# Kernel tuning notes

Hardware: AMD Instinct MI355X
Metric: run time of the kernel (lower is better)

## Reference

```python
import jax, jax.numpy as jnp
import numpy as np

N_NODES = 65536   # N
D_HID   = 128     # D (hidden)
N_GROUPS = 16384  # G portfolios
GROUP_LEN = 64    # lines per portfolio (port_len entries)
N_LINES = N_GROUPS * GROUP_LEN  # L
BATCH = 16384     # B samples


def setup_inputs() -> dict:
    key = jax.random.key(0)
    k = jax.random.split(key, 5)
    H = jax.random.normal(k[0], (N_NODES, D_HID), dtype=jnp.float32)
    port_w_signed_flat = jax.random.normal(k[1], (N_LINES,), dtype=jnp.float32)
    anchor_idx = jax.random.randint(k[2], (BATCH,), 0, N_NODES, dtype=jnp.int32)
    pf_gid = jax.random.randint(k[3], (BATCH,), 0, N_GROUPS, dtype=jnp.int32)
    port_nodes_flat = jax.random.randint(k[4], (N_LINES,), 0, N_NODES, dtype=jnp.int32)
    port_len = jnp.full((N_GROUPS,), GROUP_LEN, dtype=jnp.int32)
    return {
        'H': H,
        'port_w_signed_flat': port_w_signed_flat,
        'anchor_idx': anchor_idx,
        'pf_gid': pf_gid,
        'port_nodes_flat': port_nodes_flat,
        'port_len': port_len,
    }


def reference(H, port_w_signed_flat, anchor_idx, pf_gid, port_nodes_flat, port_len):
    """Faithful, vectorized port of compute_samplewise_portfolio_vectors_loo.

    Ragged segment-weighted mean per portfolio group, with strict leave-one-out
    correction for each sample's anchor node, followed by L2 normalization.
    Returns (V_abs, V_sgn), each [B, D].
    """
    N, D = H.shape
    G = port_len.shape[0]
    L = port_nodes_flat.shape[0]

    # gid per flat line: repeat_interleave(arange(G), lens)
    gid_lines = jnp.repeat(jnp.arange(G, dtype=jnp.int32), port_len,
                           total_repeat_length=L)

    w_abs = jnp.abs(port_w_signed_flat)
    Hl = H[port_nodes_flat]                                  # [L, D] gather
    S_abs = jax.ops.segment_sum(w_abs[:, None] * Hl, gid_lines, num_segments=G)
    W_abs = jax.ops.segment_sum(w_abs, gid_lines, num_segments=G)
    W_sgn = jax.ops.segment_sum(port_w_signed_flat, gid_lines, num_segments=G)

    valid = (pf_gid >= 0) & (pf_gid < G)
    g = jnp.clip(pf_gid, 0, G - 1)

    # Leave-one-out self-weight: sum of w over lines where (gid==g_i, node==anchor_i).
    # Vectorized join via a sorted composite int32 key (G*N < 2^31 by construction).
    keys_l = gid_lines * N + port_nodes_flat                 # [L]
    keys_s = g * N + anchor_idx                              # [B]
    order = jnp.argsort(keys_l)
    sk = keys_l[order]
    zero1 = jnp.zeros((1,), H.dtype)
    ca = jnp.concatenate([zero1, jnp.cumsum(w_abs[order])])
    cs = jnp.concatenate([zero1, jnp.cumsum(port_w_signed_flat[order])])
    lo = jnp.searchsorted(sk, keys_s, side='left')
    hi = jnp.searchsorted(sk, keys_s, side='right')
    self_w_abs = ca[hi] - ca[lo]                             # [B]
    self_w_sgn = cs[hi] - cs[lo]                             # [B]

    Ha = H[anchor_idx]                                       # [B, D]
    denom = jnp.maximum(W_abs[g] - self_w_abs, 1e-12)        # clamp_min
    V_abs = (S_abs[g] - self_w_abs[:, None] * Ha) / denom[:, None]
    V_sgn = ((W_sgn[g] - self_w_sgn) / denom)[:, None] * V_abs

    V_abs = jnp.where(valid[:, None], V_abs, jnp.zeros((), H.dtype))
    V_sgn = jnp.where(valid[:, None], V_sgn, jnp.zeros((), H.dtype))

    # torch F.normalize: x / clamp(||x||, min=eps)
    na = jnp.linalg.norm(V_abs, axis=1, keepdims=True)
    V_abs = V_abs / jnp.maximum(na, 1e-6)
    ns = jnp.linalg.norm(V_sgn, axis=1, keepdims=True)
    V_sgn = jnp.where(ns > 0, V_sgn / jnp.maximum(ns, 1e-6), V_sgn)
    return V_abs, V_sgn
```

## Files before the change

### kernel.cpp

```cpp
#include <hip/hip_runtime.h>
#include <hip/hip_bf16.h>


#define DDIM 128

__device__ inline unsigned bf_rne(float x) {
    unsigned u = __float_as_uint(x);
    return (u + 0x7FFFu + ((u >> 16) & 1u)) >> 16;
}

__device__ inline void unpack2(unsigned d, float& lo, float& hi) {
    lo = __uint_as_float(d << 16);
    hi = __uint_as_float(d & 0xFFFF0000u);
}

__global__ __launch_bounds__(1024) void init_kernel(
    const float4* __restrict__ H4, uint2* __restrict__ Hb, int n4,
    const int* __restrict__ plen, int* __restrict__ offs, int G,
    const int* __restrict__ pf_gid, int* __restrict__ used, int B, int nconv) {
    const int t = threadIdx.x;
    const int bb = blockIdx.x;
    if (bb < nconv) {
        const int i = bb * 1024 + t;
        if (i < n4) {
            const float4 v = H4[i];
            uint2 o;
            o.x = bf_rne(v.x) | (bf_rne(v.y) << 16);
            o.y = bf_rne(v.z) | (bf_rne(v.w) << 16);
            Hb[i] = o;
        }
        return;
    }
    if (bb == nconv) {
        for (int i = t; i < G; i += 1024) used[i] = 0;
        __syncthreads();
        for (int i = t; i < B; i += 1024) {
            const int g = pf_gid[i];
            if (g >= 0 && g < G) used[g] = 1;
        }
        return;
    }
    __shared__ int part[1024];
    const int chunk = (G + 1023) >> 10;
    const int lo = min(t * chunk, G);
    const int hi = min(lo + chunk, G);
    int s = 0;
    for (int i = lo; i < hi; ++i) s += plen[i];
    part[t] = s;
    __syncthreads();
    #pragma unroll
    for (int ofs = 1; ofs < 1024; ofs <<= 1) {
        int v = (t >= ofs) ? part[t - ofs] : 0;
        __syncthreads();
        part[t] += v;
        __syncthreads();
    }
    int run = part[t] - s;
    for (int i = lo; i < hi; ++i) { offs[i] = run; run += plen[i]; }
}

__global__ __launch_bounds__(256) void group_sums(
    const unsigned short* __restrict__ Hb,
    const float* __restrict__ pw, const int* __restrict__ pn,
    const int* __restrict__ plen, const int* __restrict__ offs,
    const int* __restrict__ used,
    float* __restrict__ Sabs, float* __restrict__ Wag,
    float* __restrict__ Wsg, int G) {
    const int g = blockIdx.x * (blockDim.x >> 6) + (threadIdx.x >> 6);
    const int lane = threadIdx.x & 63;
    const int q = lane >> 4;
    const int s = lane & 15;
    if (g >= G || !used[g]) return;

    const int off = offs[g];
    const int len = plen[g];

    float acc[8] = {0.f, 0.f, 0.f, 0.f, 0.f, 0.f, 0.f, 0.f};
    float laWa = 0.f, laWs = 0.f;

    for (int base = 0; base < len; base += 64) {
        const int jmax = min(64, len - base);
        float wl = 0.f;
        int nl = 0;
        if (lane < jmax) {
            wl = pw[off + base + lane];
            nl = pn[off + base + lane];
        }
        laWa += fabsf(wl);
        laWs += wl;

        #pragma unroll 8
        for (int jj = 0; jj < 64; jj += 4) {
            const float ww = fabsf(__shfl(wl, jj + q));
            const int row = __shfl(nl, jj + q);
            const uint4 h = *((const uint4*)(Hb + (size_t)row * DDIM) + s);
            float f0, f1, f2, f3, f4, f5, f6, f7;
            unpack2(h.x, f0, f1);
            unpack2(h.y, f2, f3);
            unpack2(h.z, f4, f5);
            unpack2(h.w, f6, f7);
            acc[0] = fmaf(ww, f0, acc[0]);
            acc[1] = fmaf(ww, f1, acc[1]);
            acc[2] = fmaf(ww, f2, acc[2]);
            acc[3] = fmaf(ww, f3, acc[3]);
            acc[4] = fmaf(ww, f4, acc[4]);
            acc[5] = fmaf(ww, f5, acc[5]);
            acc[6] = fmaf(ww, f6, acc[6]);
            acc[7] = fmaf(ww, f7, acc[7]);
        }
    }

    #pragma unroll
    for (int m = 32; m; m >>= 1) {
        laWa += __shfl_xor(laWa, m);
        laWs += __shfl_xor(laWs, m);
    }
    #pragma unroll
    for (int k = 0; k < 8; ++k) {
        acc[k] += __shfl_xor(acc[k], 16);
        acc[k] += __shfl_xor(acc[k], 32);
    }

    if (q == 0) {
        float4* dst = (float4*)(Sabs + (size_t)g * DDIM);
        dst[2 * s] = make_float4(acc[0], acc[1], acc[2], acc[3]);
        dst[2 * s + 1] = make_float4(acc[4], acc[5], acc[6], acc[7]);
    }
    if (lane == 0) { Wag[g] = laWa; Wsg[g] = laWs; }
}

__global__ __launch_bounds__(256) void per_sample(
    const unsigned short* __restrict__ Hb,
    const float* __restrict__ pw, const int* __restrict__ pn,
    const int* __restrict__ plen, const int* __restrict__ offs,
    const float* __restrict__ Sabs, const float* __restrict__ Wag,
    const float* __restrict__ Wsg,
    const int* __restrict__ anchor_idx, const int* __restrict__ pf_gid,
    float* __restrict__ out, int B, int G) {
    const int b = blockIdx.x * (blockDim.x >> 6) + (threadIdx.x >> 6);
    const int lane = threadIdx.x & 63;
    if (b >= B) return;

    float2* outA = (float2*)(out + (size_t)b * DDIM);
    float2* outS = (float2*)(out + ((size_t)B + b) * DDIM);

    const int g = pf_gid[b];
    if (!(g >= 0 && g < G)) {
        const float2 z = make_float2(0.f, 0.f);
        outA[lane] = z;
        outS[lane] = z;
        return;
    }

    const int anchor = anchor_idx[b];
    const int off = offs[g];
    const int len = plen[g];

    float selfa = 0.f, selfs = 0.f;
    for (int base = 0; base < len; base += 64) {
        const int jmax = min(64, len - base);
        if (lane < jmax) {
            const float w = pw[off + base + lane];
            const int n = pn[off + base + lane];
            if (n == anchor) { selfa += fabsf(w); selfs += w; }
        }
    }
    #pragma unroll
    for (int m = 32; m; m >>= 1) {
        selfa += __shfl_xor(selfa, m);
        selfs += __shfl_xor(selfs, m);
    }

    const float Wa = Wag[g];
    const float Wsn = Wsg[g];
    const float2 S = ((const float2*)(Sabs + (size_t)g * DDIM))[lane];
    const unsigned hb = *((const unsigned*)(Hb + (size_t)anchor * DDIM) + lane);
    float h0, h1;
    unpack2(hb, h0, h1);

    const float denom = fmaxf(Wa - selfa, 1e-12f);
    float2 v;
    v.x = (S.x - selfa * h0) / denom;
    v.y = (S.y - selfa * h1) / denom;
    const float scale = (Wsn - selfs) / denom;

    float n2 = v.x * v.x + v.y * v.y;
    #pragma unroll
    for (int m = 32; m; m >>= 1) n2 += __shfl_xor(n2, m);
    const float na = sqrtf(n2);

    const float invA = 1.0f / fmaxf(na, 1e-6f);
    const float ns = fabsf(scale) * na;
    const float sgnscale = (ns > 0.f) ? (scale / fmaxf(ns, 1e-6f)) : scale;

    outA[lane] = make_float2(v.x * invA, v.y * invA);
    outS[lane] = make_float2(v.x * sgnscale, v.y * sgnscale);
}

__global__ __launch_bounds__(1024) void scan_only(
    const int* __restrict__ len, int* __restrict__ offs, int G) {
    __shared__ int part[1024];
    const int t = threadIdx.x;
    const int chunk = (G + 1023) >> 10;
    const int lo = min(t * chunk, G);
    const int hi = min(lo + chunk, G);
    int s = 0;
    for (int i = lo; i < hi; ++i) s += len[i];
    part[t] = s;
    __syncthreads();
    #pragma unroll
    for (int ofs = 1; ofs < 1024; ofs <<= 1) {
        int v = (t >= ofs) ? part[t - ofs] : 0;
        __syncthreads();
        part[t] += v;
        __syncthreads();
    }
    int run = part[t] - s;
    for (int i = lo; i < hi; ++i) { offs[i] = run; run += len[i]; }
}

__global__ __launch_bounds__(256) void pf_loo_f32(
    const float* __restrict__ H, const float* __restrict__ pw,
    const int* __restrict__ anchor_idx, const int* __restrict__ pf_gid,
    const int* __restrict__ pn, const int* __restrict__ plen,
    const int* __restrict__ offs, float* __restrict__ out, int B, int G) {
    const int b = blockIdx.x * (blockDim.x >> 6) + (threadIdx.x >> 6);
    const int lane = threadIdx.x & 63;
    const int half = lane >> 5;
    const int qlane = lane & 31;
    if (b >= B) return;
    float4* outA = (float4*)(out + (size_t)b * DDIM);
    float4* outS = (float4*)(out + ((size_t)B + b) * DDIM);
    const int gid = pf_gid[b];
    if (!(gid >= 0 && gid < G)) {
        float4 z = make_float4(0.f, 0.f, 0.f, 0.f);
        if (half == 0) { outA[qlane] = z; outS[qlane] = z; }
        return;
    }
    const int anchor = anchor_idx[b];
    const int off = offs[gid];
    const int len = plen[gid];
    float4 acc = make_float4(0.f, 0.f, 0.f, 0.f);
    float laWa = 0.f, laWs = 0.f, laSa = 0.f, laSs = 0.f;
    for (int base = 0; base < len; base += 64) {
        const int jmax = min(64, len - base);
        float wl = 0.f;
        int nl = 0;
        if (lane < jmax) { wl = pw[off + base + lane]; nl = pn[off + base + lane]; }
        const float wla = fabsf(wl);
        laWa += wla; laWs += wl;
        if (nl == anchor) { laSa += wla; laSs += wl; }
        #pragma unroll 8
        for (int jj = 0; jj < 64; jj += 2) {
            const float ww = fabsf(__shfl(wl, jj + half));
            const int row = __shfl(nl, jj + half);
            const float4 h = ((const float4*)(H + (size_t)row * DDIM))[qlane];
            acc.x = fmaf(ww, h.x, acc.x);
            acc.y = fmaf(ww, h.y, acc.y);
            acc.z = fmaf(ww, h.z, acc.z);
            acc.w = fmaf(ww, h.w, acc.w);
        }
    }
    #pragma unroll
    for (int m = 32; m; m >>= 1) {
        laWa += __shfl_xor(laWa, m);
        laWs += __shfl_xor(laWs, m);
        laSa += __shfl_xor(laSa, m);
        laSs += __shfl_xor(laSs, m);
    }
    acc.x += __shfl_xor(acc.x, 32);
    acc.y += __shfl_xor(acc.y, 32);
    acc.z += __shfl_xor(acc.z, 32);
    acc.w += __shfl_xor(acc.w, 32);
    const float denom = fmaxf(laWa - laSa, 1e-12f);
    const float4 hv = ((const float4*)(H + (size_t)anchor * DDIM))[qlane];
    float4 v;
    v.x = (acc.x - laSa * hv.x) / denom;
    v.y = (acc.y - laSa * hv.y) / denom;
    v.z = (acc.z - laSa * hv.z) / denom;
    v.w = (acc.w - laSa * hv.w) / denom;
    const float scale = (laWs - laSs) / denom;
    float n2 = v.x * v.x + v.y * v.y + v.z * v.z + v.w * v.w;
    #pragma unroll
    for (int m = 32; m; m >>= 1) n2 += __shfl_xor(n2, m);
    n2 *= 0.5f;
    const float na = sqrtf(n2);
    const float invA = 1.0f / fmaxf(na, 1e-6f);
    const float ns = fabsf(scale) * na;
    const float sgnscale = (ns > 0.f) ? (scale / fmaxf(ns, 1e-6f)) : scale;
    const float sc = half ? sgnscale : invA;
    float4 res = make_float4(v.x * sc, v.y * sc, v.z * sc, v.w * sc);
    float4* dst = half ? outS : outA;
    dst[qlane] = res;
}

extern "C" void kernel_launch(void* const* d_in, const int* in_sizes, int n_in,
                              void* d_out, int out_size, void* d_ws, size_t ws_size,
                              hipStream_t stream) {
    const float* H      = (const float*)d_in[0];
    const float* pw     = (const float*)d_in[1];
    const int* anchor   = (const int*)d_in[2];
    const int* gid      = (const int*)d_in[3];
    const int* pn       = (const int*)d_in[4];
    const int* plen     = (const int*)d_in[5];
    float* out          = (float*)d_out;

    const int B = in_sizes[2];
    const int G = in_sizes[5];
    const int ND = in_sizes[0];
    const size_t hb_bytes = (size_t)ND * 2;
    const size_t sabs_bytes = (size_t)G * DDIM * 4;
    const size_t need = hb_bytes + sabs_bytes + (size_t)G * 4 * 4;

    if (ws_size >= need) {
        char* p = (char*)d_ws;
        unsigned short* Hb = (unsigned short*)p;        p += hb_bytes;
        float* Sabs        = (float*)p;                 p += sabs_bytes;
        int* offsp         = (int*)p;                   p += (size_t)G * 4;
        int* usedp         = (int*)p;                   p += (size_t)G * 4;
        float* Wag         = (float*)p;                 p += (size_t)G * 4;
        float* Wsg         = (float*)p;

        const int n4 = ND / 4;
        const int nconv = (n4 + 1023) / 1024;
        init_kernel<<<nconv + 2, 1024, 0, stream>>>(
            (const float4*)H, (uint2*)Hb, n4, plen, offsp, G, gid, usedp, B, nconv);

        const int gblocks = (G + 3) / 4;
        group_sums<<<gblocks, 256, 0, stream>>>(Hb, pw, pn, plen, offsp, usedp,
                                                Sabs, Wag, Wsg, G);

        const int sblocks = (B + 3) / 4;
        per_sample<<<sblocks, 256, 0, stream>>>(Hb, pw, pn, plen, offsp, Sabs,
                                                Wag, Wsg, anchor, gid, out, B, G);
    } else {
        int* offsp = (int*)d_ws;
        scan_only<<<1, 1024, 0, stream>>>(plen, offsp, G);
        const int blocks = (B + 3) / 4;
        pf_loo_f32<<<blocks, 256, 0, stream>>>(H, pw, anchor, gid, pn, plen,
                                               offsp, out, B, G);
    }
}
```

Measured before the change: 142.6 us.

## Fuse group sums and per-sample LOO output via bucketed sample lists

Replaces the per-sample kernel by bucketing samples per group in the init kernel (LDS histogram, scan, and scatter into a sample list) and computing each sample's leave-one-out output inside the group kernel. This removes the Sabs/Wag/Wsg round trip through global memory, one kernel launch, and the second pass over line weights for the self-weight. The trade-off is that the bucketing runs in a single 1024-thread block, each wave carries per-sample registers for up to 8 samples, and groups with more than 8 samples fall back to a serial loop.

```diff
diff --git a/kernel.cpp b/kernel.cpp
--- a/kernel.cpp
+++ b/kernel.cpp
@@ -3,6 +3,8 @@
 
 
 #define DDIM 128
+#define SMAX 8
+#define MAXG_LDS 16384
 
 __device__ inline unsigned bf_rne(float x) {
     unsigned u = __float_as_uint(x);
@@ -17,9 +19,12 @@
 __global__ __launch_bounds__(1024) void init_kernel(
     const float4* __restrict__ H4, uint2* __restrict__ Hb, int n4,
     const int* __restrict__ plen, int* __restrict__ offs, int G,
-    const int* __restrict__ pf_gid, int* __restrict__ used, int B, int nconv) {
+    const int* __restrict__ pf_gid, int* __restrict__ sstart,
+    int* __restrict__ slist, float* __restrict__ out, int B, int nconv) {
+    __shared__ int shm[MAXG_LDS];
     const int t = threadIdx.x;
     const int bb = blockIdx.x;
+
     if (bb < nconv) {
         const int i = bb * 1024 + t;
         if (i < n4) {
@@ -31,63 +36,134 @@
         }
         return;
     }
+
     if (bb == nconv) {
-        for (int i = t; i < G; i += 1024) used[i] = 0;
+        for (int i = t; i < G; i += 1024) shm[i] = 0;
         __syncthreads();
         for (int i = t; i < B; i += 1024) {
             const int g = pf_gid[i];
-            if (g >= 0 && g < G) used[g] = 1;
+            if (g >= 0 && g < G) {
+                atomicAdd(&shm[g], 1);
+            } else {
+                float4* oa = (float4*)(out + (size_t)i * DDIM);
+                float4* os = (float4*)(out + ((size_t)B + i) * DDIM);
+                const float4 z = make_float4(0.f, 0.f, 0.f, 0.f);
+                for (int k = 0; k < DDIM / 4; ++k) { oa[k] = z; os[k] = z; }
+            }
+        }
+        __syncthreads();
+        const int chunk = (G + 1023) >> 10;
+        int c[16];
+        int local = 0;
+        #pragma unroll
+        for (int k = 0; k < 16; ++k) {
+            const int idx = t * chunk + k;
+            c[k] = (k < chunk && idx < G) ? shm[idx] : 0;
+            local += c[k];
+        }
+        __syncthreads();
+        const int lane = t & 63, wid = t >> 6;
+        int incl = local;
+        #pragma unroll
+        for (int m = 1; m < 64; m <<= 1) {
+            int v = __shfl_up(incl, m);
+            if (lane >= m) incl += v;
+        }
+        if (lane == 63) shm[wid] = incl;
+        __syncthreads();
+        int woff = 0;
+        for (int i = 0; i < wid; ++i) woff += shm[i];
+        const int excl = woff + incl - local;
+        __syncthreads();
+        int run = excl;
+        #pragma unroll
+        for (int k = 0; k < 16; ++k) {
+            const int idx = t * chunk + k;
+            if (k < chunk && idx < G) {
+                sstart[idx] = run;
+                shm[idx] = run;
+                run += c[k];
+            }
+        }
+        if (t == 1023) sstart[G] = run;
+        __syncthreads();
+        for (int i = t; i < B; i += 1024) {
+            const int g = pf_gid[i];
+            if (g >= 0 && g < G) {
+                const int pos = atomicAdd(&shm[g], 1);
+                slist[pos] = i;
+            }
         }
         return;
     }
-    __shared__ int part[1024];
+
     const int chunk = (G + 1023) >> 10;
     const int lo = min(t * chunk, G);
     const int hi = min(lo + chunk, G);
     int s = 0;
     for (int i = lo; i < hi; ++i) s += plen[i];
-    part[t] = s;
+    shm[t] = s;
     __syncthreads();
     #pragma unroll
     for (int ofs = 1; ofs < 1024; ofs <<= 1) {
-        int v = (t >= ofs) ? part[t - ofs] : 0;
-        __syncthreads();
-        part[t] += v;
-        __syncthreads();
-    }
-    int run = part[t] - s;
+        int v = (t >= ofs) ? shm[t - ofs] : 0;
+        __syncthreads();
+        shm[t] += v;
+        __syncthreads();
+    }
+    int run = shm[t] - s;
     for (int i = lo; i < hi; ++i) { offs[i] = run; run += plen[i]; }
 }
 
-__global__ __launch_bounds__(256) void group_sums(
+__global__ __launch_bounds__(256) void group_fused(
     const unsigned short* __restrict__ Hb,
     const float* __restrict__ pw, const int* __restrict__ pn,
     const int* __restrict__ plen, const int* __restrict__ offs,
-    const int* __restrict__ used,
-    float* __restrict__ Sabs, float* __restrict__ Wag,
-    float* __restrict__ Wsg, int G) {
+    const int* __restrict__ sstart, const int* __restrict__ slist,
+    const int* __restrict__ anchor_idx,
+    float* __restrict__ out, int B, int G) {
     const int g = blockIdx.x * (blockDim.x >> 6) + (threadIdx.x >> 6);
     const int lane = threadIdx.x & 63;
     const int q = lane >> 4;
     const int s = lane & 15;
-    if (g >= G || !used[g]) return;
+    if (g >= G) return;
+
+    const int slo = sstart[g];
+    const int shi = sstart[g + 1];
+    const int count = shi - slo;
+    if (count == 0) return;
 
     const int off = offs[g];
     const int len = plen[g];
 
+    int sid[SMAX], anc[SMAX];
+    #pragma unroll
+    for (int i = 0; i < SMAX; ++i) {
+        sid[i] = (i < count) ? slist[slo + i] : -1;
+        anc[i] = (sid[i] >= 0) ? anchor_idx[sid[i]] : -1;
+    }
+
     float acc[8] = {0.f, 0.f, 0.f, 0.f, 0.f, 0.f, 0.f, 0.f};
+    float selfa[SMAX], selfs[SMAX];
+    #pragma unroll
+    for (int i = 0; i < SMAX; ++i) { selfa[i] = 0.f; selfs[i] = 0.f; }
     float laWa = 0.f, laWs = 0.f;
 
     for (int base = 0; base < len; base += 64) {
         const int jmax = min(64, len - base);
         float wl = 0.f;
-        int nl = 0;
+        int nl = -1;
         if (lane < jmax) {
             wl = pw[off + base + lane];
             nl = pn[off + base + lane];
         }
-        laWa += fabsf(wl);
+        const float wla = fabsf(wl);
+        laWa += wla;
         laWs += wl;
+        #pragma unroll
+        for (int i = 0; i < SMAX; ++i) {
+            if (nl == anc[i]) { selfa[i] += wla; selfs[i] += wl; }
+        }
 
         #pragma unroll 8
         for (int jj = 0; jj < 64; jj += 4) {
@@ -116,85 +192,110 @@
         laWs += __shfl_xor(laWs, m);
     }
     #pragma unroll
+    for (int i = 0; i < SMAX; ++i) {
+        if (i < count) {
+            #pragma unroll
+            for (int m = 32; m; m >>= 1) {
+                selfa[i] += __shfl_xor(selfa[i], m);
+                selfs[i] += __shfl_xor(selfs[i], m);
+            }
+        }
+    }
+    #pragma unroll
     for (int k = 0; k < 8; ++k) {
         acc[k] += __shfl_xor(acc[k], 16);
         acc[k] += __shfl_xor(acc[k], 32);
     }
 
-    if (q == 0) {
-        float4* dst = (float4*)(Sabs + (size_t)g * DDIM);
-        dst[2 * s] = make_float4(acc[0], acc[1], acc[2], acc[3]);
-        dst[2 * s + 1] = make_float4(acc[4], acc[5], acc[6], acc[7]);
-    }
-    if (lane == 0) { Wag[g] = laWa; Wsg[g] = laWs; }
-}
-
-__global__ __launch_bounds__(256) void per_sample(
-    const unsigned short* __restrict__ Hb,
-    const float* __restrict__ pw, const int* __restrict__ pn,
-    const int* __restrict__ plen, const int* __restrict__ offs,
-    const float* __restrict__ Sabs, const float* __restrict__ Wag,
-    const float* __restrict__ Wsg,
-    const int* __restrict__ anchor_idx, const int* __restrict__ pf_gid,
-    float* __restrict__ out, int B, int G) {
-    const int b = blockIdx.x * (blockDim.x >> 6) + (threadIdx.x >> 6);
-    const int lane = threadIdx.x & 63;
-    if (b >= B) return;
-
-    float2* outA = (float2*)(out + (size_t)b * DDIM);
-    float2* outS = (float2*)(out + ((size_t)B + b) * DDIM);
-
-    const int g = pf_gid[b];
-    if (!(g >= 0 && g < G)) {
-        const float2 z = make_float2(0.f, 0.f);
-        outA[lane] = z;
-        outS[lane] = z;
-        return;
-    }
-
-    const int anchor = anchor_idx[b];
-    const int off = offs[g];
-    const int len = plen[g];
-
-    float selfa = 0.f, selfs = 0.f;
-    for (int base = 0; base < len; base += 64) {
-        const int jmax = min(64, len - base);
-        if (lane < jmax) {
-            const float w = pw[off + base + lane];
-            const int n = pn[off + base + lane];
-            if (n == anchor) { selfa += fabsf(w); selfs += w; }
-        }
-    }
-    #pragma unroll
-    for (int m = 32; m; m >>= 1) {
-        selfa += __shfl_xor(selfa, m);
-        selfs += __shfl_xor(selfs, m);
-    }
-
-    const float Wa = Wag[g];
-    const float Wsn = Wsg[g];
-    const float2 S = ((const float2*)(Sabs + (size_t)g * DDIM))[lane];
-    const unsigned hb = *((const unsigned*)(Hb + (size_t)anchor * DDIM) + lane);
-    float h0, h1;
-    unpack2(hb, h0, h1);
-
-    const float denom = fmaxf(Wa - selfa, 1e-12f);
-    float2 v;
-    v.x = (S.x - selfa * h0) / denom;
-    v.y = (S.y - selfa * h1) / denom;
-    const float scale = (Wsn - selfs) / denom;
-
-    float n2 = v.x * v.x + v.y * v.y;
-    #pragma unroll
-    for (int m = 32; m; m >>= 1) n2 += __shfl_xor(n2, m);
-    const float na = sqrtf(n2);
-
-    const float invA = 1.0f / fmaxf(na, 1e-6f);
-    const float ns = fabsf(scale) * na;
-    const float sgnscale = (ns > 0.f) ? (scale / fmaxf(ns, 1e-6f)) : scale;
-
-    outA[lane] = make_float2(v.x * invA, v.y * invA);
-    outS[lane] = make_float2(v.x * sgnscale, v.y * sgnscale);
+    const int nmain = min(count, SMAX);
+    for (int i = 0; i < nmain; ++i) {
+        const int sb = sid[i];
+        const float sa = selfa[i], ss = selfs[i];
+        const float denom = fmaxf(laWa - sa, 1e-12f);
+        const float scale = (laWs - ss) / denom;
+
+        const uint4 ha = *((const uint4*)(Hb + (size_t)anc[i] * DDIM) + s);
+        float hv[8];
+        unpack2(ha.x, hv[0], hv[1]);
+        unpack2(ha.y, hv[2], hv[3]);
+        unpack2(ha.z, hv[4], hv[5]);
+        unpack2(ha.w, hv[6], hv[7]);
+
+        float v[8];
+        float n2 = 0.f;
+        #pragma unroll
+        for (int k = 0; k < 8; ++k) {
+            v[k] = (acc[k] - sa * hv[k]) / denom;
+            n2 = fmaf(v[k], v[k], n2);
+        }
+        #pragma unroll
+        for (int m = 32; m; m >>= 1) n2 += __shfl_xor(n2, m);
+        n2 *= 0.25f;
+        const float na = sqrtf(n2);
+        const float invA = 1.0f / fmaxf(na, 1e-6f);
+        const float ns = fabsf(scale) * na;
+        const float sgnscale = (ns > 0.f) ? (scale / fmaxf(ns, 1e-6f)) : scale;
+
+        if (q == 0) {
+            float4* oa = (float4*)(out + (size_t)sb * DDIM);
+            oa[2 * s] = make_float4(v[0] * invA, v[1] * invA, v[2] * invA, v[3] * invA);
+            oa[2 * s + 1] = make_float4(v[4] * invA, v[5] * invA, v[6] * invA, v[7] * invA);
+        } else if (q == 1) {
+            float4* os = (float4*)(out + ((size_t)B + sb) * DDIM);
+            os[2 * s] = make_float4(v[0] * sgnscale, v[1] * sgnscale, v[2] * sgnscale, v[3] * sgnscale);
+            os[2 * s + 1] = make_float4(v[4] * sgnscale, v[5] * sgnscale, v[6] * sgnscale, v[7] * sgnscale);
+        }
+    }
+
+    for (int i = SMAX; i < count; ++i) {
+        const int sb = slist[slo + i];
+        const int an = anchor_idx[sb];
+        float sa = 0.f, ss = 0.f;
+        for (int base = 0; base < len; base += 64) {
+            const int jmax = min(64, len - base);
+            if (lane < jmax) {
+                const float w = pw[off + base + lane];
+                const int n = pn[off + base + lane];
+                if (n == an) { sa += fabsf(w); ss += w; }
+            }
+        }
+        #pragma unroll
+        for (int m = 32; m; m >>= 1) {
+            sa += __shfl_xor(sa, m);
+            ss += __shfl_xor(ss, m);
+        }
+        const float denom = fmaxf(laWa - sa, 1e-12f);
+        const float scale = (laWs - ss) / denom;
+        const uint4 ha = *((const uint4*)(Hb + (size_t)an * DDIM) + s);
+        float hv[8];
+        unpack2(ha.x, hv[0], hv[1]);
+        unpack2(ha.y, hv[2], hv[3]);
+        unpack2(ha.z, hv[4], hv[5]);
+        unpack2(ha.w, hv[6], hv[7]);
+        float v[8];
+        float n2 = 0.f;
+        #pragma unroll
+        for (int k = 0; k < 8; ++k) {
+            v[k] = (acc[k] - sa * hv[k]) / denom;
+            n2 = fmaf(v[k], v[k], n2);
+        }
+        #pragma unroll
+        for (int m = 32; m; m >>= 1) n2 += __shfl_xor(n2, m);
+        n2 *= 0.25f;
+        const float na = sqrtf(n2);
+        const float invA = 1.0f / fmaxf(na, 1e-6f);
+        const float ns = fabsf(scale) * na;
+        const float sgnscale = (ns > 0.f) ? (scale / fmaxf(ns, 1e-6f)) : scale;
+        if (q == 0) {
+            float4* oa = (float4*)(out + (size_t)sb * DDIM);
+            oa[2 * s] = make_float4(v[0] * invA, v[1] * invA, v[2] * invA, v[3] * invA);
+            oa[2 * s + 1] = make_float4(v[4] * invA, v[5] * invA, v[6] * invA, v[7] * invA);
+        } else if (q == 1) {
+            float4* os = (float4*)(out + ((size_t)B + sb) * DDIM);
+            os[2 * s] = make_float4(v[0] * sgnscale, v[1] * sgnscale, v[2] * sgnscale, v[3] * sgnscale);
+            os[2 * s + 1] = make_float4(v[4] * sgnscale, v[5] * sgnscale, v[6] * sgnscale, v[7] * sgnscale);
+        }
+    }
 }
 
 __global__ __launch_bounds__(1024) void scan_only(
@@ -245,7 +346,7 @@
     for (int base = 0; base < len; base += 64) {
         const int jmax = min(64, len - base);
         float wl = 0.f;
-        int nl = 0;
+        int nl = -1;
         if (lane < jmax) { wl = pw[off + base + lane]; nl = pn[off + base + lane]; }
         const float wla = fabsf(wl);
         laWa += wla; laWs += wl;
@@ -309,30 +410,26 @@
     const int G = in_sizes[5];
     const int ND = in_sizes[0];
     const size_t hb_bytes = (size_t)ND * 2;
-    const size_t sabs_bytes = (size_t)G * DDIM * 4;
-    const size_t need = hb_bytes + sabs_bytes + (size_t)G * 4 * 4;
-
-    if (ws_size >= need) {
+    const size_t need = hb_bytes + (size_t)(G + 1) * 4 + (size_t)B * 4 +
+                        (size_t)G * 4;
+
+    if (ws_size >= need && G <= MAXG_LDS) {
         char* p = (char*)d_ws;
-        unsigned short* Hb = (unsigned short*)p;        p += hb_bytes;
-        float* Sabs        = (float*)p;                 p += sabs_bytes;
-        int* offsp         = (int*)p;                   p += (size_t)G * 4;
-        int* usedp         = (int*)p;                   p += (size_t)G * 4;
-        float* Wag         = (float*)p;                 p += (size_t)G * 4;
-        float* Wsg         = (float*)p;
+        unsigned short* Hb = (unsigned short*)p;  p += hb_bytes;
+        int* sstart        = (int*)p;             p += (size_t)(G + 1) * 4;
+        int* slist         = (int*)p;             p += (size_t)B * 4;
+        int* offsp         = (int*)p;
 
         const int n4 = ND / 4;
         const int nconv = (n4 + 1023) / 1024;
         init_kernel<<<nconv + 2, 1024, 0, stream>>>(
-            (const float4*)H, (uint2*)Hb, n4, plen, offsp, G, gid, usedp, B, nconv);
+            (const float4*)H, (uint2*)Hb, n4, plen, offsp, G, gid,
+            sstart, slist, out, B, nconv);
 
         const int gblocks = (G + 3) / 4;
-        group_sums<<<gblocks, 256, 0, stream>>>(Hb, pw, pn, plen, offsp, usedp,
-                                                Sabs, Wag, Wsg, G);
-
-        const int sblocks = (B + 3) / 4;
-        per_sample<<<sblocks, 256, 0, stream>>>(Hb, pw, pn, plen, offsp, Sabs,
-                                                Wag, Wsg, anchor, gid, out, B, G);
+        group_fused<<<gblocks, 256, 0, stream>>>(Hb, pw, pn, plen, offsp,
+                                                 sstart, slist, anchor,
+                                                 out, B, G);
     } else {
         int* offsp = (int*)d_ws;
         scan_only<<<1, 1024, 0, stream>>>(plen, offsp, G);
```

Result: slower. 155.8 us (+9.2%).

## Split each group's line reduction across two wavefronts with LDS combine

Applied to the files above, without the earlier changes.

group_sums now launches one 128-thread block per group instead of one wavefront per group. Each wave handles 32 of the 64 lines, and the partial sums are combined through shared memory before being written to Sabs. The goal is twice as many wavefronts and a shorter dependent gather chain per wave, which should hide more of the random-row gather latency. The cost is a __syncthreads, an LDS round trip, and partly idle lanes during the line loads. A separate fallback-path fix initialises nl to -1 so padded lanes cannot match anchor 0.

```diff
diff --git a/kernel.cpp b/kernel.cpp
--- a/kernel.cpp
+++ b/kernel.cpp
@@ -59,18 +59,23 @@
     for (int i = lo; i < hi; ++i) { offs[i] = run; run += plen[i]; }
 }
 
-__global__ __launch_bounds__(256) void group_sums(
+__global__ __launch_bounds__(128) void group_sums(
     const unsigned short* __restrict__ Hb,
     const float* __restrict__ pw, const int* __restrict__ pn,
     const int* __restrict__ plen, const int* __restrict__ offs,
     const int* __restrict__ used,
     float* __restrict__ Sabs, float* __restrict__ Wag,
     float* __restrict__ Wsg, int G) {
-    const int g = blockIdx.x * (blockDim.x >> 6) + (threadIdx.x >> 6);
-    const int lane = threadIdx.x & 63;
+    const int g = blockIdx.x;
+    if (g >= G || !used[g]) return;
+    const int tid = threadIdx.x;
+    const int wid = tid >> 6;
+    const int lane = tid & 63;
     const int q = lane >> 4;
     const int s = lane & 15;
-    if (g >= G || !used[g]) return;
+
+    __shared__ float ldsS[2][DDIM];
+    __shared__ float ldsW[4];
 
     const int off = offs[g];
     const int len = plen[g];
@@ -79,18 +84,18 @@
     float laWa = 0.f, laWs = 0.f;
 
     for (int base = 0; base < len; base += 64) {
-        const int jmax = min(64, len - base);
+        const int l0 = base + wid * 32;
         float wl = 0.f;
         int nl = 0;
-        if (lane < jmax) {
-            wl = pw[off + base + lane];
-            nl = pn[off + base + lane];
+        if (lane < 32 && l0 + lane < len) {
+            wl = pw[off + l0 + lane];
+            nl = pn[off + l0 + lane];
         }
         laWa += fabsf(wl);
         laWs += wl;
 
-        #pragma unroll 8
-        for (int jj = 0; jj < 64; jj += 4) {
+        #pragma unroll
+        for (int jj = 0; jj < 32; jj += 4) {
             const float ww = fabsf(__shfl(wl, jj + q));
             const int row = __shfl(nl, jj + q);
             const uint4 h = *((const uint4*)(Hb + (size_t)row * DDIM) + s);
@@ -122,11 +127,19 @@
     }
 
     if (q == 0) {
-        float4* dst = (float4*)(Sabs + (size_t)g * DDIM);
-        dst[2 * s] = make_float4(acc[0], acc[1], acc[2], acc[3]);
-        dst[2 * s + 1] = make_float4(acc[4], acc[5], acc[6], acc[7]);
-    }
-    if (lane == 0) { Wag[g] = laWa; Wsg[g] = laWs; }
+        #pragma unroll
+        for (int k = 0; k < 8; ++k) ldsS[wid][8 * s + k] = acc[k];
+    }
+    if (lane == 0) { ldsW[wid] = laWa; ldsW[2 + wid] = laWs; }
+    __syncthreads();
+
+    if (tid < DDIM) {
+        Sabs[(size_t)g * DDIM + tid] = ldsS[0][tid] + ldsS[1][tid];
+    }
+    if (tid == 0) {
+        Wag[g] = ldsW[0] + ldsW[1];
+        Wsg[g] = ldsW[2] + ldsW[3];
+    }
 }
 
 __global__ __launch_bounds__(256) void per_sample(
@@ -245,7 +258,7 @@
     for (int base = 0; base < len; base += 64) {
         const int jmax = min(64, len - base);
         float wl = 0.f;
-        int nl = 0;
+        int nl = -1;
         if (lane < jmax) { wl = pw[off + base + lane]; nl = pn[off + base + lane]; }
         const float wla = fabsf(wl);
         laWa += wla; laWs += wl;
@@ -326,9 +339,8 @@
         init_kernel<<<nconv + 2, 1024, 0, stream>>>(
             (const float4*)H, (uint2*)Hb, n4, plen, offsp, G, gid, usedp, B, nconv);
 
-        const int gblocks = (G + 3) / 4;
-        group_sums<<<gblocks, 256, 0, stream>>>(Hb, pw, pn, plen, offsp, usedp,
-                                                Sabs, Wag, Wsg, G);
+        group_sums<<<G, 128, 0, stream>>>(Hb, pw, pn, plen, offsp, usedp,
+                                          Sabs, Wag, Wsg, G);
 
         const int sblocks = (B + 3) / 4;
         per_sample<<<sblocks, 256, 0, stream>>>(Hb, pw, pn, plen, offsp, Sabs,
```

Result: no change. 142.6 us (-0.0%).
